# Kernel optimization log

Measured on AMD Instinct MI355X. Metric: run time of the kernel, lower is better.

## Reference

```python
import jax, jax.numpy as jnp
import numpy as np

N_NODES = 50000
N_EDGES = 800000
NUM_GRAPHS = 512
IN_DIM = 128
HID = 128
OUT_DIM = 1


def setup_inputs() -> dict:
    key = jax.random.key(0)
    ks = jax.random.split(key, 8)
    x = jax.random.normal(ks[0], (N_NODES, IN_DIM), dtype=jnp.float32)
    edge_index = jax.random.randint(ks[1], (2, N_EDGES), 0, N_NODES, dtype=jnp.int64)
    batch = jnp.sort(jax.random.randint(ks[2], (N_NODES,), 0, NUM_GRAPHS, dtype=jnp.int64))
    s1 = 1.0 / np.sqrt(IN_DIM)
    s2 = 1.0 / np.sqrt(HID)
    W1 = jax.random.normal(ks[3], (IN_DIM, HID), dtype=jnp.float32) * s1
    b1 = jnp.zeros((HID,), dtype=jnp.float32)
    W2 = jax.random.normal(ks[4], (HID, HID), dtype=jnp.float32) * s2
    b2 = jnp.zeros((HID,), dtype=jnp.float32)
    Wl = jax.random.normal(ks[5], (HID, OUT_DIM), dtype=jnp.float32) * s2
    bl = jnp.zeros((OUT_DIM,), dtype=jnp.float32)
    return {"x": x, "edge_index": edge_index, "batch": batch,
            "W1": W1, "b1": b1, "W2": W2, "b2": b2, "Wl": Wl, "bl": bl}


def _gcn_conv(x, src, dst, norm, W, b):
    # GCNConv: D^{-1/2}(A+I)D^{-1/2} X W + b (self-loops already in src/dst)
    h = x @ W                                    # [N, H]
    msg = h[src] * norm[:, None]                 # gather + edge-normalize
    agg = jax.ops.segment_sum(msg, dst, num_segments=N_NODES)  # scatter-add
    return agg + b


def reference(x, edge_index, batch, W1, b1, W2, b2, Wl, bl):
    loops = jnp.arange(N_NODES, dtype=edge_index.dtype)
    src = jnp.concatenate([edge_index[0], loops])
    dst = jnp.concatenate([edge_index[1], loops])
    deg = jax.ops.segment_sum(jnp.ones_like(dst, dtype=x.dtype), dst, num_segments=N_NODES)
    dinv = jax.lax.rsqrt(deg)                    # deg >= 1 due to self-loops
    norm = dinv[src] * dinv[dst]                 # symmetric normalization per edge

    h = jax.nn.relu(_gcn_conv(x, src, dst, norm, W1, b1))
    h = jax.nn.relu(_gcn_conv(h, src, dst, norm, W2, b2))

    # global_mean_pool over graph ids
    sums = jax.ops.segment_sum(h, batch, num_segments=NUM_GRAPHS)
    cnts = jax.ops.segment_sum(jnp.ones((N_NODES,), dtype=h.dtype), batch, num_segments=NUM_GRAPHS)
    pooled = sums / jnp.maximum(cnts, 1.0)[:, None]

    out = jax.nn.sigmoid(pooled @ Wl + bl)       # [G, 1]
    return out.squeeze(1)                        # [G]
```

## Files before the change

### kernel.cpp

```cpp
#include <hip/hip_runtime.h>
#include <hip/hip_bf16.h>

#define N_NODES 50000
#define N_EDGES 800000
#define NUM_GRAPHS 512
#define MAXDEG 64
#define EPB 4096
#define P1_BLOCKS 196
#define NBUCK 256
#define NPB 196

typedef short short8 __attribute__((ext_vector_type(8)));
typedef unsigned short u16x8 __attribute__((ext_vector_type(8)));
typedef float f32x4 __attribute__((ext_vector_type(4)));

__device__ __forceinline__ unsigned short f2bu(float f) {
    __hip_bfloat16 h = __float2bfloat16(f);
    return *reinterpret_cast<unsigned short*>(&h);
}
__device__ __forceinline__ float bu2f(unsigned short u) {
    unsigned int v = ((unsigned int)u) << 16;
    float f;
    __builtin_memcpy(&f, &v, 4);
    return f;
}

__global__ __launch_bounds__(256) void bin_k(const int* __restrict__ ei,
                                             unsigned int* __restrict__ staging,
                                             int* __restrict__ cnts_tbl,
                                             int* __restrict__ offs_tbl,
                                             unsigned short* __restrict__ hs1,
                                             unsigned short* __restrict__ hs2) {
    __shared__ unsigned int st[EPB];
    __shared__ int cnt[NBUCK], cur[NBUCK], scan[NBUCK];
    int b = blockIdx.x, t = threadIdx.x;
    if (b == 0 && t < 64)
        ((unsigned int*)(hs1 + (size_t)N_NODES * 128))[t] = 0u;
    if (b == 1 && t < 64)
        ((unsigned int*)(hs2 + (size_t)N_NODES * 128))[t] = 0u;
    cnt[t] = 0;
    __syncthreads();

    int e0 = b * EPB;
    int srcv[16], dstv[16], bk[16];
#pragma unroll
    for (int k = 0; k < 16; ++k) {
        int e = e0 + k * 256 + t;
        bool ok = e < N_EDGES;
        srcv[k] = ok ? ei[e] : 0;
        dstv[k] = ok ? ei[N_EDGES + e] : 0;
        bk[k] = ok ? (dstv[k] / NPB) : -1;
        if (ok) atomicAdd(&cnt[bk[k]], 1);
    }
    __syncthreads();
    scan[t] = cnt[t];
    __syncthreads();
    for (int off = 1; off < 256; off <<= 1) {
        int u = t >= off ? scan[t - off] : 0;
        __syncthreads();
        scan[t] += u;
        __syncthreads();
    }
    int excl = scan[t] - cnt[t];
    cur[t] = excl;
    cnts_tbl[t * P1_BLOCKS + b] = cnt[t];
    offs_tbl[t * P1_BLOCKS + b] = excl;
    __syncthreads();
#pragma unroll
    for (int k = 0; k < 16; ++k) {
        if (bk[k] >= 0) {
            int pos = atomicAdd(&cur[bk[k]], 1);
            int dl = dstv[k] - bk[k] * NPB;
            st[pos] = (unsigned int)srcv[k] | ((unsigned int)dl << 16);
        }
    }
    __syncthreads();
    unsigned int* gout = staging + (size_t)b * EPB;
    for (int i = t; i < EPB; i += 256) gout[i] = st[i];
}

__global__ __launch_bounds__(256) void adjbuild_k(const unsigned int* __restrict__ staging,
                                                  const int* __restrict__ cnts_tbl,
                                                  const int* __restrict__ offs_tbl,
                                                  unsigned short* __restrict__ adj,
                                                  int* __restrict__ cnt,
                                                  float* __restrict__ dinv,
                                                  const float* __restrict__ W1,
                                                  const float* __restrict__ W2,
                                                  unsigned short* __restrict__ W1t,
                                                  unsigned short* __restrict__ W2t) {
    int b = blockIdx.x, t = threadIdx.x;
    if (b >= NBUCK) {
        int wb = b - NBUCK;
        const float* W = wb < 64 ? W1 : W2;
        unsigned short* Wt = wb < 64 ? W1t : W2t;
        int idx = (wb & 63) * 256 + t;
        int k = idx >> 7, n = idx & 127;
        Wt[n * 128 + k] = f2bu(W[idx]);
        return;
    }
    __shared__ unsigned short adjL[NPB * MAXDEG];
    __shared__ int cntL[NPB];
    __shared__ int segStart[P1_BLOCKS + 1];
    __shared__ int segOff[P1_BLOCKS];
    __shared__ int tmp[256];

    if (t < NPB) cntL[t] = 0;
    int c = t < P1_BLOCKS ? cnts_tbl[b * P1_BLOCKS + t] : 0;
    if (t < P1_BLOCKS) segOff[t] = offs_tbl[b * P1_BLOCKS + t];
    tmp[t] = c;
    __syncthreads();
    for (int off = 1; off < 256; off <<= 1) {
        int u = t >= off ? tmp[t - off] : 0;
        __syncthreads();
        tmp[t] += u;
        __syncthreads();
    }
    if (t < P1_BLOCKS) segStart[t] = tmp[t] - c;
    if (t == 0) segStart[P1_BLOCKS] = tmp[P1_BLOCKS - 1];
    __syncthreads();

    int T = segStart[P1_BLOCKS];
    for (int f = t; f < T; f += 256) {
        int lo = 0, hi = P1_BLOCKS;
        while (hi - lo > 1) {
            int m = (lo + hi) >> 1;
            if (segStart[m] <= f) lo = m; else hi = m;
        }
        unsigned int p = staging[(size_t)lo * EPB + segOff[lo] + (f - segStart[lo])];
        int src = p & 0xFFFF;
        int dl = p >> 16;
        int slot = atomicAdd(&cntL[dl], 1);
        if (slot < MAXDEG - 1) adjL[dl * MAXDEG + slot] = (unsigned short)src;
    }
    __syncthreads();

    int nodeBase = b * NPB;
    if (t < NPB) {
        int node = nodeBase + t;
        int cc = cntL[t];
        int ec = cc < MAXDEG - 1 ? cc : MAXDEG - 1;
        adjL[t * MAXDEG + ec] = (unsigned short)node;
        int tot = ec + 1, tot4 = (tot + 3) & ~3;
        for (int s = tot; s < tot4; ++s) adjL[t * MAXDEG + s] = (unsigned short)N_NODES;
        if (node < N_NODES) {
            cnt[node] = cc;
            dinv[node] = rsqrtf((float)cc + 1.0f);
        }
    }
    __syncthreads();
    unsigned int* g = (unsigned int*)(adj + (size_t)nodeBase * MAXDEG);
    const unsigned int* l = (const unsigned int*)adjL;
    for (int i = t; i < NPB * MAXDEG / 2; i += 256) g[i] = l[i];
}

template <bool F32A>
__global__ __launch_bounds__(256) void gemm_k(const void* __restrict__ Ap,
                                              const unsigned short* __restrict__ Wt,
                                              const float* __restrict__ dinv,
                                              unsigned short* __restrict__ C) {
    __shared__ unsigned short Wl[128 * 136];
    int t = threadIdx.x;
    for (int idx = t; idx < 2048; idx += 256) {
        int n = idx >> 4, c = idx & 15;
        *(u16x8*)(Wl + n * 136 + c * 8) = *(const u16x8*)(Wt + n * 128 + c * 8);
    }
    __syncthreads();

    int wave = t >> 6, lane = t & 63, quad = lane >> 4, ln = lane & 15;
    int rb = blockIdx.x * 128 + wave * 16;

    short8 a[2][4];
#pragma unroll
    for (int mt = 0; mt < 2; ++mt) {
        int r = rb + mt * 64 + ln;
        r = r < N_NODES ? r : N_NODES - 1;
        if (F32A) {
            const float* arow = (const float*)Ap + (size_t)r * 128 + quad * 8;
#pragma unroll
            for (int ks = 0; ks < 4; ++ks) {
                float4 v0 = *(const float4*)(arow + ks * 32);
                float4 v1 = *(const float4*)(arow + ks * 32 + 4);
                short8 av;
                av[0] = (short)f2bu(v0.x); av[1] = (short)f2bu(v0.y);
                av[2] = (short)f2bu(v0.z); av[3] = (short)f2bu(v0.w);
                av[4] = (short)f2bu(v1.x); av[5] = (short)f2bu(v1.y);
                av[6] = (short)f2bu(v1.z); av[7] = (short)f2bu(v1.w);
                a[mt][ks] = av;
            }
        } else {
            const unsigned short* arow = (const unsigned short*)Ap + (size_t)r * 128 + quad * 8;
#pragma unroll
            for (int ks = 0; ks < 4; ++ks) a[mt][ks] = *(const short8*)(arow + ks * 32);
        }
    }

    f32x4 acc[2][8];
#pragma unroll
    for (int mt = 0; mt < 2; ++mt)
#pragma unroll
        for (int ct = 0; ct < 8; ++ct) acc[mt][ct] = (f32x4){0.f, 0.f, 0.f, 0.f};

#pragma unroll
    for (int ks = 0; ks < 4; ++ks)
#pragma unroll
        for (int ct = 0; ct < 8; ++ct) {
            short8 b = *(const short8*)(Wl + (ct * 16 + ln) * 136 + ks * 32 + quad * 8);
            acc[0][ct] = __builtin_amdgcn_mfma_f32_16x16x32_bf16(a[0][ks], b, acc[0][ct], 0, 0, 0);
            acc[1][ct] = __builtin_amdgcn_mfma_f32_16x16x32_bf16(a[1][ks], b, acc[1][ct], 0, 0, 0);
        }

#pragma unroll
    for (int mt = 0; mt < 2; ++mt) {
#pragma unroll
        for (int rr = 0; rr < 4; ++rr) {
            int r = rb + mt * 64 + quad * 4 + rr;
            if (r >= N_NODES) continue;
            float dv = dinv[r];
#pragma unroll
            for (int ct = 0; ct < 8; ++ct)
                C[(size_t)r * 128 + ct * 16 + ln] = f2bu(acc[mt][ct][rr] * dv);
        }
    }
}

__global__ __launch_bounds__(256) void agg1_k(const unsigned short* __restrict__ hs,
                                              const unsigned short* __restrict__ adj,
                                              const int* __restrict__ cnt,
                                              const float* __restrict__ dinv,
                                              const float* __restrict__ bias,
                                              unsigned short* __restrict__ out) {
    int wave = threadIdx.x >> 6, lane = threadIdx.x & 63;
    int node0 = blockIdx.x * 8 + wave * 2;
    int node1 = node0 + 1;
    int quad = lane >> 4, fl = lane & 15;
    int idx0 = (int)adj[node0 * MAXDEG + lane];
    int idx1 = (int)adj[node1 * MAXDEG + lane];
    int c0 = cnt[node0], c1 = cnt[node1];
    int ec0 = c0 < MAXDEG - 1 ? c0 : MAXDEG - 1;
    int ec1 = c1 < MAXDEG - 1 ? c1 : MAXDEG - 1;
    int it0 = (ec0 + 4) >> 2;
    int it1 = (ec1 + 4) >> 2;
    int common = it0 < it1 ? it0 : it1;

    float a0[8], a1[8];
#pragma unroll
    for (int j = 0; j < 8; ++j) { a0[j] = 0.f; a1[j] = 0.f; }

    int i = 0;
    for (; i + 2 <= common; i += 2) {
        int sA0 = __shfl(idx0, i * 4 + quad, 64);
        int sA1 = __shfl(idx0, i * 4 + 4 + quad, 64);
        int sB0 = __shfl(idx1, i * 4 + quad, 64);
        int sB1 = __shfl(idx1, i * 4 + 4 + quad, 64);
        u16x8 vA0 = *(const u16x8*)(hs + (size_t)sA0 * 128 + fl * 8);
        u16x8 vA1 = *(const u16x8*)(hs + (size_t)sA1 * 128 + fl * 8);
        u16x8 vB0 = *(const u16x8*)(hs + (size_t)sB0 * 128 + fl * 8);
        u16x8 vB1 = *(const u16x8*)(hs + (size_t)sB1 * 128 + fl * 8);
#pragma unroll
        for (int j = 0; j < 8; ++j) {
            a0[j] += bu2f(vA0[j]) + bu2f(vA1[j]);
            a1[j] += bu2f(vB0[j]) + bu2f(vB1[j]);
        }
    }
    for (; i < common; ++i) {
        int sA = __shfl(idx0, i * 4 + quad, 64);
        int sB = __shfl(idx1, i * 4 + quad, 64);
        u16x8 vA = *(const u16x8*)(hs + (size_t)sA * 128 + fl * 8);
        u16x8 vB = *(const u16x8*)(hs + (size_t)sB * 128 + fl * 8);
#pragma unroll
        for (int j = 0; j < 8; ++j) { a0[j] += bu2f(vA[j]); a1[j] += bu2f(vB[j]); }
    }
    for (; i < it0; ++i) {
        int sA = __shfl(idx0, i * 4 + quad, 64);
        u16x8 vA = *(const u16x8*)(hs + (size_t)sA * 128 + fl * 8);
#pragma unroll
        for (int j = 0; j < 8; ++j) a0[j] += bu2f(vA[j]);
    }
    for (; i < it1; ++i) {
        int sB = __shfl(idx1, i * 4 + quad, 64);
        u16x8 vB = *(const u16x8*)(hs + (size_t)sB * 128 + fl * 8);
#pragma unroll
        for (int j = 0; j < 8; ++j) a1[j] += bu2f(vB[j]);
    }

#pragma unroll
    for (int j = 0; j < 8; ++j) {
        a0[j] += __shfl_xor(a0[j], 16, 64);
        a0[j] += __shfl_xor(a0[j], 32, 64);
        a1[j] += __shfl_xor(a1[j], 16, 64);
        a1[j] += __shfl_xor(a1[j], 32, 64);
    }

    if (quad < 2) {
        int node = quad == 0 ? node0 : node1;
        const float* av = nullptr;
        float dv = dinv[node];
        float4 b0 = *(const float4*)(bias + fl * 8);
        float4 b1 = *(const float4*)(bias + fl * 8 + 4);
        float r0 = quad == 0 ? a0[0] : a1[0];
        float r1 = quad == 0 ? a0[1] : a1[1];
        float r2 = quad == 0 ? a0[2] : a1[2];
        float r3 = quad == 0 ? a0[3] : a1[3];
        float r4 = quad == 0 ? a0[4] : a1[4];
        float r5 = quad == 0 ? a0[5] : a1[5];
        float r6 = quad == 0 ? a0[6] : a1[6];
        float r7 = quad == 0 ? a0[7] : a1[7];
        u16x8 o;
        o[0] = f2bu(fmaxf(r0 * dv + b0.x, 0.f));
        o[1] = f2bu(fmaxf(r1 * dv + b0.y, 0.f));
        o[2] = f2bu(fmaxf(r2 * dv + b0.z, 0.f));
        o[3] = f2bu(fmaxf(r3 * dv + b0.w, 0.f));
        o[4] = f2bu(fmaxf(r4 * dv + b1.x, 0.f));
        o[5] = f2bu(fmaxf(r5 * dv + b1.y, 0.f));
        o[6] = f2bu(fmaxf(r6 * dv + b1.z, 0.f));
        o[7] = f2bu(fmaxf(r7 * dv + b1.w, 0.f));
        *(u16x8*)(out + (size_t)node * 128 + fl * 8) = o;
        (void)av;
    }
}

__global__ __launch_bounds__(256) void agg_dot_k(const unsigned short* __restrict__ hs,
                                                 const unsigned short* __restrict__ adj,
                                                 const int* __restrict__ cnt,
                                                 const float* __restrict__ dinv,
                                                 const float* __restrict__ bias,
                                                 const float* __restrict__ Wl,
                                                 float* __restrict__ pnode) {
    int wave = threadIdx.x >> 6, lane = threadIdx.x & 63;
    int node0 = blockIdx.x * 8 + wave * 2;
    int node1 = node0 + 1;
    int quad = lane >> 4, fl = lane & 15;
    int idx0 = (int)adj[node0 * MAXDEG + lane];
    int idx1 = (int)adj[node1 * MAXDEG + lane];
    int c0 = cnt[node0], c1 = cnt[node1];
    int ec0 = c0 < MAXDEG - 1 ? c0 : MAXDEG - 1;
    int ec1 = c1 < MAXDEG - 1 ? c1 : MAXDEG - 1;
    int it0 = (ec0 + 4) >> 2;
    int it1 = (ec1 + 4) >> 2;
    int common = it0 < it1 ? it0 : it1;

    float a0[8], a1[8];
#pragma unroll
    for (int j = 0; j < 8; ++j) { a0[j] = 0.f; a1[j] = 0.f; }

    int i = 0;
    for (; i + 2 <= common; i += 2) {
        int sA0 = __shfl(idx0, i * 4 + quad, 64);
        int sA1 = __shfl(idx0, i * 4 + 4 + quad, 64);
        int sB0 = __shfl(idx1, i * 4 + quad, 64);
        int sB1 = __shfl(idx1, i * 4 + 4 + quad, 64);
        u16x8 vA0 = *(const u16x8*)(hs + (size_t)sA0 * 128 + fl * 8);
        u16x8 vA1 = *(const u16x8*)(hs + (size_t)sA1 * 128 + fl * 8);
        u16x8 vB0 = *(const u16x8*)(hs + (size_t)sB0 * 128 + fl * 8);
        u16x8 vB1 = *(const u16x8*)(hs + (size_t)sB1 * 128 + fl * 8);
#pragma unroll
        for (int j = 0; j < 8; ++j) {
            a0[j] += bu2f(vA0[j]) + bu2f(vA1[j]);
            a1[j] += bu2f(vB0[j]) + bu2f(vB1[j]);
        }
    }
    for (; i < common; ++i) {
        int sA = __shfl(idx0, i * 4 + quad, 64);
        int sB = __shfl(idx1, i * 4 + quad, 64);
        u16x8 vA = *(const u16x8*)(hs + (size_t)sA * 128 + fl * 8);
        u16x8 vB = *(const u16x8*)(hs + (size_t)sB * 128 + fl * 8);
#pragma unroll
        for (int j = 0; j < 8; ++j) { a0[j] += bu2f(vA[j]); a1[j] += bu2f(vB[j]); }
    }
    for (; i < it0; ++i) {
        int sA = __shfl(idx0, i * 4 + quad, 64);
        u16x8 vA = *(const u16x8*)(hs + (size_t)sA * 128 + fl * 8);
#pragma unroll
        for (int j = 0; j < 8; ++j) a0[j] += bu2f(vA[j]);
    }
    for (; i < it1; ++i) {
        int sB = __shfl(idx1, i * 4 + quad, 64);
        u16x8 vB = *(const u16x8*)(hs + (size_t)sB * 128 + fl * 8);
#pragma unroll
        for (int j = 0; j < 8; ++j) a1[j] += bu2f(vB[j]);
    }

#pragma unroll
    for (int j = 0; j < 8; ++j) {
        a0[j] += __shfl_xor(a0[j], 16, 64);
        a0[j] += __shfl_xor(a0[j], 32, 64);
        a1[j] += __shfl_xor(a1[j], 16, 64);
        a1[j] += __shfl_xor(a1[j], 32, 64);
    }

    float dv0 = dinv[node0], dv1 = dinv[node1];
    float4 b0 = *(const float4*)(bias + fl * 8);
    float4 b1 = *(const float4*)(bias + fl * 8 + 4);
    float4 w0 = *(const float4*)(Wl + fl * 8);
    float4 w1 = *(const float4*)(Wl + fl * 8 + 4);
    float p0 = fmaxf(a0[0] * dv0 + b0.x, 0.f) * w0.x
             + fmaxf(a0[1] * dv0 + b0.y, 0.f) * w0.y
             + fmaxf(a0[2] * dv0 + b0.z, 0.f) * w0.z
             + fmaxf(a0[3] * dv0 + b0.w, 0.f) * w0.w
             + fmaxf(a0[4] * dv0 + b1.x, 0.f) * w1.x
             + fmaxf(a0[5] * dv0 + b1.y, 0.f) * w1.y
             + fmaxf(a0[6] * dv0 + b1.z, 0.f) * w1.z
             + fmaxf(a0[7] * dv0 + b1.w, 0.f) * w1.w;
    float p1 = fmaxf(a1[0] * dv1 + b0.x, 0.f) * w0.x
             + fmaxf(a1[1] * dv1 + b0.y, 0.f) * w0.y
             + fmaxf(a1[2] * dv1 + b0.z, 0.f) * w0.z
             + fmaxf(a1[3] * dv1 + b0.w, 0.f) * w0.w
             + fmaxf(a1[4] * dv1 + b1.x, 0.f) * w1.x
             + fmaxf(a1[5] * dv1 + b1.y, 0.f) * w1.y
             + fmaxf(a1[6] * dv1 + b1.z, 0.f) * w1.z
             + fmaxf(a1[7] * dv1 + b1.w, 0.f) * w1.w;
    p0 += __shfl_xor(p0, 1, 64);
    p0 += __shfl_xor(p0, 2, 64);
    p0 += __shfl_xor(p0, 4, 64);
    p0 += __shfl_xor(p0, 8, 64);
    p1 += __shfl_xor(p1, 1, 64);
    p1 += __shfl_xor(p1, 2, 64);
    p1 += __shfl_xor(p1, 4, 64);
    p1 += __shfl_xor(p1, 8, 64);
    if (lane == 0) {
        float2 pw; pw.x = p0; pw.y = p1;
        *(float2*)(pnode + node0) = pw;
    }
}

__device__ __forceinline__ int lb(const int* a, int n, int v) {
    int lo = 0, hi = n;
    while (lo < hi) {
        int m = (lo + hi) >> 1;
        if (a[m] < v) lo = m + 1;
        else hi = m;
    }
    return lo;
}

__global__ __launch_bounds__(64) void final_k(const float* __restrict__ pnode,
                                              const int* __restrict__ batch,
                                              const float* __restrict__ bl,
                                              float* __restrict__ out) {
    int g = blockIdx.x, t = threadIdx.x;
    int lo = lb(batch, N_NODES, g), hi = lb(batch, N_NODES, g + 1);
    float s = 0.f;
    for (int r = lo + t; r < hi; r += 64) s += pnode[r];
#pragma unroll
    for (int o = 32; o > 0; o >>= 1) s += __shfl_down(s, o, 64);
    if (t == 0) {
        float cf = (float)(hi - lo);
        float z = s / fmaxf(cf, 1.f) + bl[0];
        out[g] = 1.f / (1.f + expf(-z));
    }
}

extern "C" void kernel_launch(void* const* d_in, const int* in_sizes, int n_in,
                              void* d_out, int out_size, void* d_ws, size_t ws_size,
                              hipStream_t stream) {
    const float* x = (const float*)d_in[0];
    const int* ei = (const int*)d_in[1];
    const int* batch = (const int*)d_in[2];
    const float* W1 = (const float*)d_in[3];
    const float* b1 = (const float*)d_in[4];
    const float* W2 = (const float*)d_in[5];
    const float* b2 = (const float*)d_in[6];
    const float* Wl = (const float*)d_in[7];
    const float* bl = (const float*)d_in[8];
    float* out = (float*)d_out;

    char* ws = (char*)d_ws;
    unsigned int* staging = (unsigned int*)(ws + 0x0);
    int* cnts_tbl = (int*)(ws + 0x310000);
    int* offs_tbl = (int*)(ws + 0x341000);
    unsigned short* adj = (unsigned short*)(ws + 0x372000);
    int* cnt = (int*)(ws + 0x992000);
    float* dinv = (float*)(ws + 0x9C3000);
    unsigned short* W1t = (unsigned short*)(ws + 0x9F4000);
    unsigned short* W2t = (unsigned short*)(ws + 0x9FC000);
    float* pnode = (float*)(ws + 0xA04000);
    unsigned short* hs1 = (unsigned short*)(ws + 0xA36000);
    unsigned short* h1 = (unsigned short*)(ws + 0x1672000);
    unsigned short* hs2 = (unsigned short*)(ws + 0x22AE000);

    bin_k<<<P1_BLOCKS, 256, 0, stream>>>(ei, staging, cnts_tbl, offs_tbl, hs1, hs2);
    adjbuild_k<<<NBUCK + 128, 256, 0, stream>>>(staging, cnts_tbl, offs_tbl,
                                                adj, cnt, dinv, W1, W2, W1t, W2t);

    gemm_k<true><<<(N_NODES + 127) / 128, 256, 0, stream>>>(x, W1t, dinv, hs1);
    agg1_k<<<N_NODES / 8, 256, 0, stream>>>(hs1, adj, cnt, dinv, b1, h1);
    gemm_k<false><<<(N_NODES + 127) / 128, 256, 0, stream>>>(h1, W2t, dinv, hs2);
    agg_dot_k<<<N_NODES / 8, 256, 0, stream>>>(hs2, adj, cnt, dinv, b2, Wl, pnode);

    final_k<<<NUM_GRAPHS, 64, 0, stream>>>(pnode, batch, bl, out);
}
```

Measured before the change: 189.3 us.

## Reorder layer-2 as aggregate-then-GEMM and fuse W2 matmul into aggregation kernel

```diff
diff --git a/kernel.cpp b/kernel.cpp
--- a/kernel.cpp
+++ b/kernel.cpp
@@ -30,14 +30,14 @@
                                              int* __restrict__ cnts_tbl,
                                              int* __restrict__ offs_tbl,
                                              unsigned short* __restrict__ hs1,
-                                             unsigned short* __restrict__ hs2) {
+                                             unsigned short* __restrict__ h1s) {
     __shared__ unsigned int st[EPB];
     __shared__ int cnt[NBUCK], cur[NBUCK], scan[NBUCK];
     int b = blockIdx.x, t = threadIdx.x;
     if (b == 0 && t < 64)
         ((unsigned int*)(hs1 + (size_t)N_NODES * 128))[t] = 0u;
     if (b == 1 && t < 64)
-        ((unsigned int*)(hs2 + (size_t)N_NODES * 128))[t] = 0u;
+        ((unsigned int*)(h1s + (size_t)N_NODES * 128))[t] = 0u;
     cnt[t] = 0;
     __syncthreads();
 
@@ -154,8 +154,7 @@
     for (int i = t; i < NPB * MAXDEG / 2; i += 256) g[i] = l[i];
 }
 
-template <bool F32A>
-__global__ __launch_bounds__(256) void gemm_k(const void* __restrict__ Ap,
+__global__ __launch_bounds__(256) void gemm_k(const float* __restrict__ Ap,
                                               const unsigned short* __restrict__ Wt,
                                               const float* __restrict__ dinv,
                                               unsigned short* __restrict__ C) {
@@ -175,23 +174,17 @@
     for (int mt = 0; mt < 2; ++mt) {
         int r = rb + mt * 64 + ln;
         r = r < N_NODES ? r : N_NODES - 1;
-        if (F32A) {
-            const float* arow = (const float*)Ap + (size_t)r * 128 + quad * 8;
-#pragma unroll
-            for (int ks = 0; ks < 4; ++ks) {
-                float4 v0 = *(const float4*)(arow + ks * 32);
-                float4 v1 = *(const float4*)(arow + ks * 32 + 4);
-                short8 av;
-                av[0] = (short)f2bu(v0.x); av[1] = (short)f2bu(v0.y);
-                av[2] = (short)f2bu(v0.z); av[3] = (short)f2bu(v0.w);
-                av[4] = (short)f2bu(v1.x); av[5] = (short)f2bu(v1.y);
-                av[6] = (short)f2bu(v1.z); av[7] = (short)f2bu(v1.w);
-                a[mt][ks] = av;
-            }
-        } else {
-            const unsigned short* arow = (const unsigned short*)Ap + (size_t)r * 128 + quad * 8;
-#pragma unroll
-            for (int ks = 0; ks < 4; ++ks) a[mt][ks] = *(const short8*)(arow + ks * 32);
+        const float* arow = Ap + (size_t)r * 128 + quad * 8;
+#pragma unroll
+        for (int ks = 0; ks < 4; ++ks) {
+            float4 v0 = *(const float4*)(arow + ks * 32);
+            float4 v1 = *(const float4*)(arow + ks * 32 + 4);
+            short8 av;
+            av[0] = (short)f2bu(v0.x); av[1] = (short)f2bu(v0.y);
+            av[2] = (short)f2bu(v0.z); av[3] = (short)f2bu(v0.w);
+            av[4] = (short)f2bu(v1.x); av[5] = (short)f2bu(v1.y);
+            av[6] = (short)f2bu(v1.z); av[7] = (short)f2bu(v1.w);
+            a[mt][ks] = av;
         }
     }
 
@@ -294,7 +287,6 @@
 
     if (quad < 2) {
         int node = quad == 0 ? node0 : node1;
-        const float* av = nullptr;
         float dv = dinv[node];
         float4 b0 = *(const float4*)(bias + fl * 8);
         float4 b1 = *(const float4*)(bias + fl * 8 + 4);
@@ -307,30 +299,36 @@
         float r6 = quad == 0 ? a0[6] : a1[6];
         float r7 = quad == 0 ? a0[7] : a1[7];
         u16x8 o;
-        o[0] = f2bu(fmaxf(r0 * dv + b0.x, 0.f));
-        o[1] = f2bu(fmaxf(r1 * dv + b0.y, 0.f));
-        o[2] = f2bu(fmaxf(r2 * dv + b0.z, 0.f));
-        o[3] = f2bu(fmaxf(r3 * dv + b0.w, 0.f));
-        o[4] = f2bu(fmaxf(r4 * dv + b1.x, 0.f));
-        o[5] = f2bu(fmaxf(r5 * dv + b1.y, 0.f));
-        o[6] = f2bu(fmaxf(r6 * dv + b1.z, 0.f));
-        o[7] = f2bu(fmaxf(r7 * dv + b1.w, 0.f));
+        o[0] = f2bu(fmaxf(r0 * dv + b0.x, 0.f) * dv);
+        o[1] = f2bu(fmaxf(r1 * dv + b0.y, 0.f) * dv);
+        o[2] = f2bu(fmaxf(r2 * dv + b0.z, 0.f) * dv);
+        o[3] = f2bu(fmaxf(r3 * dv + b0.w, 0.f) * dv);
+        o[4] = f2bu(fmaxf(r4 * dv + b1.x, 0.f) * dv);
+        o[5] = f2bu(fmaxf(r5 * dv + b1.y, 0.f) * dv);
+        o[6] = f2bu(fmaxf(r6 * dv + b1.z, 0.f) * dv);
+        o[7] = f2bu(fmaxf(r7 * dv + b1.w, 0.f) * dv);
         *(u16x8*)(out + (size_t)node * 128 + fl * 8) = o;
-        (void)av;
-    }
-}
-
-__global__ __launch_bounds__(256) void agg_dot_k(const unsigned short* __restrict__ hs,
-                                                 const unsigned short* __restrict__ adj,
-                                                 const int* __restrict__ cnt,
-                                                 const float* __restrict__ dinv,
-                                                 const float* __restrict__ bias,
-                                                 const float* __restrict__ Wl,
-                                                 float* __restrict__ pnode) {
-    int wave = threadIdx.x >> 6, lane = threadIdx.x & 63;
-    int node0 = blockIdx.x * 8 + wave * 2;
-    int node1 = node0 + 1;
+    }
+}
+
+__global__ __launch_bounds__(256) void agg_w2_dot_k(const unsigned short* __restrict__ h1s,
+                                                    const unsigned short* __restrict__ adj,
+                                                    const int* __restrict__ cnt,
+                                                    const float* __restrict__ dinv,
+                                                    const float* __restrict__ b2,
+                                                    const float* __restrict__ Wl,
+                                                    const unsigned short* __restrict__ W2t,
+                                                    float* __restrict__ pnode) {
+    __shared__ unsigned short tA[16 * 136];
+    __shared__ float part[8][4];
+    int t = threadIdx.x, wave = t >> 6, lane = t & 63;
     int quad = lane >> 4, fl = lane & 15;
+    int nb = blockIdx.x * 8;
+    int node0 = nb + wave * 2, node1 = node0 + 1;
+
+    for (int i = t; i < 544; i += 256)
+        ((unsigned int*)(tA + 8 * 136))[i] = 0u;
+
     int idx0 = (int)adj[node0 * MAXDEG + lane];
     int idx1 = (int)adj[node1 * MAXDEG + lane];
     int c0 = cnt[node0], c1 = cnt[node1];
@@ -350,10 +348,10 @@
         int sA1 = __shfl(idx0, i * 4 + 4 + quad, 64);
         int sB0 = __shfl(idx1, i * 4 + quad, 64);
         int sB1 = __shfl(idx1, i * 4 + 4 + quad, 64);
-        u16x8 vA0 = *(const u16x8*)(hs + (size_t)sA0 * 128 + fl * 8);
-        u16x8 vA1 = *(const u16x8*)(hs + (size_t)sA1 * 128 + fl * 8);
-        u16x8 vB0 = *(const u16x8*)(hs + (size_t)sB0 * 128 + fl * 8);
-        u16x8 vB1 = *(const u16x8*)(hs + (size_t)sB1 * 128 + fl * 8);
+        u16x8 vA0 = *(const u16x8*)(h1s + (size_t)sA0 * 128 + fl * 8);
+        u16x8 vA1 = *(const u16x8*)(h1s + (size_t)sA1 * 128 + fl * 8);
+        u16x8 vB0 = *(const u16x8*)(h1s + (size_t)sB0 * 128 + fl * 8);
+        u16x8 vB1 = *(const u16x8*)(h1s + (size_t)sB1 * 128 + fl * 8);
 #pragma unroll
         for (int j = 0; j < 8; ++j) {
             a0[j] += bu2f(vA0[j]) + bu2f(vA1[j]);
@@ -363,20 +361,20 @@
     for (; i < common; ++i) {
         int sA = __shfl(idx0, i * 4 + quad, 64);
         int sB = __shfl(idx1, i * 4 + quad, 64);
-        u16x8 vA = *(const u16x8*)(hs + (size_t)sA * 128 + fl * 8);
-        u16x8 vB = *(const u16x8*)(hs + (size_t)sB * 128 + fl * 8);
+        u16x8 vA = *(const u16x8*)(h1s + (size_t)sA * 128 + fl * 8);
+        u16x8 vB = *(const u16x8*)(h1s + (size_t)sB * 128 + fl * 8);
 #pragma unroll
         for (int j = 0; j < 8; ++j) { a0[j] += bu2f(vA[j]); a1[j] += bu2f(vB[j]); }
     }
     for (; i < it0; ++i) {
         int sA = __shfl(idx0, i * 4 + quad, 64);
-        u16x8 vA = *(const u16x8*)(hs + (size_t)sA * 128 + fl * 8);
+        u16x8 vA = *(const u16x8*)(h1s + (size_t)sA * 128 + fl * 8);
 #pragma unroll
         for (int j = 0; j < 8; ++j) a0[j] += bu2f(vA[j]);
     }
     for (; i < it1; ++i) {
         int sB = __shfl(idx1, i * 4 + quad, 64);
-        u16x8 vB = *(const u16x8*)(hs + (size_t)sB * 128 + fl * 8);
+        u16x8 vB = *(const u16x8*)(h1s + (size_t)sB * 128 + fl * 8);
 #pragma unroll
         for (int j = 0; j < 8; ++j) a1[j] += bu2f(vB[j]);
     }
@@ -389,39 +387,58 @@
         a1[j] += __shfl_xor(a1[j], 32, 64);
     }
 
-    float dv0 = dinv[node0], dv1 = dinv[node1];
-    float4 b0 = *(const float4*)(bias + fl * 8);
-    float4 b1 = *(const float4*)(bias + fl * 8 + 4);
-    float4 w0 = *(const float4*)(Wl + fl * 8);
-    float4 w1 = *(const float4*)(Wl + fl * 8 + 4);
-    float p0 = fmaxf(a0[0] * dv0 + b0.x, 0.f) * w0.x
-             + fmaxf(a0[1] * dv0 + b0.y, 0.f) * w0.y
-             + fmaxf(a0[2] * dv0 + b0.z, 0.f) * w0.z
-             + fmaxf(a0[3] * dv0 + b0.w, 0.f) * w0.w
-             + fmaxf(a0[4] * dv0 + b1.x, 0.f) * w1.x
-             + fmaxf(a0[5] * dv0 + b1.y, 0.f) * w1.y
-             + fmaxf(a0[6] * dv0 + b1.z, 0.f) * w1.z
-             + fmaxf(a0[7] * dv0 + b1.w, 0.f) * w1.w;
-    float p1 = fmaxf(a1[0] * dv1 + b0.x, 0.f) * w0.x
-             + fmaxf(a1[1] * dv1 + b0.y, 0.f) * w0.y
-             + fmaxf(a1[2] * dv1 + b0.z, 0.f) * w0.z
-             + fmaxf(a1[3] * dv1 + b0.w, 0.f) * w0.w
-             + fmaxf(a1[4] * dv1 + b1.x, 0.f) * w1.x
-             + fmaxf(a1[5] * dv1 + b1.y, 0.f) * w1.y
-             + fmaxf(a1[6] * dv1 + b1.z, 0.f) * w1.z
-             + fmaxf(a1[7] * dv1 + b1.w, 0.f) * w1.w;
-    p0 += __shfl_xor(p0, 1, 64);
-    p0 += __shfl_xor(p0, 2, 64);
-    p0 += __shfl_xor(p0, 4, 64);
-    p0 += __shfl_xor(p0, 8, 64);
-    p1 += __shfl_xor(p1, 1, 64);
-    p1 += __shfl_xor(p1, 2, 64);
-    p1 += __shfl_xor(p1, 4, 64);
-    p1 += __shfl_xor(p1, 8, 64);
-    if (lane == 0) {
-        float2 pw; pw.x = p0; pw.y = p1;
-        *(float2*)(pnode + node0) = pw;
-    }
+    if (quad < 2) {
+        u16x8 o;
+#pragma unroll
+        for (int j = 0; j < 8; ++j) o[j] = f2bu(quad == 0 ? a0[j] : a1[j]);
+        *(u16x8*)(tA + (wave * 2 + quad) * 136 + fl * 8) = o;
+    }
+    __syncthreads();
+
+    int ln = fl;
+    short8 af[4];
+#pragma unroll
+    for (int ks = 0; ks < 4; ++ks)
+        af[ks] = *(const short8*)(tA + ln * 136 + ks * 32 + quad * 8);
+
+    f32x4 acc2[2];
+    acc2[0] = (f32x4){0.f, 0.f, 0.f, 0.f};
+    acc2[1] = (f32x4){0.f, 0.f, 0.f, 0.f};
+#pragma unroll
+    for (int ks = 0; ks < 4; ++ks)
+#pragma unroll
+        for (int ct = 0; ct < 2; ++ct) {
+            short8 bf = *(const short8*)(W2t + (size_t)(wave * 32 + ct * 16 + ln) * 128 + ks * 32 + quad * 8);
+            acc2[ct] = __builtin_amdgcn_mfma_f32_16x16x32_bf16(af[ks], bf, acc2[ct], 0, 0, 0);
+        }
+
+    float dvr[4];
+#pragma unroll
+    for (int rr = 0; rr < 4; ++rr) {
+        int nidx = nb + quad * 4 + rr;
+        nidx = nidx < N_NODES ? nidx : N_NODES - 1;
+        dvr[rr] = dinv[nidx];
+    }
+    float b2v[2], wlv[2];
+#pragma unroll
+    for (int ct = 0; ct < 2; ++ct) {
+        int col = wave * 32 + ct * 16 + ln;
+        b2v[ct] = b2[col];
+        wlv[ct] = Wl[col];
+    }
+#pragma unroll
+    for (int rr = 0; rr < 4; ++rr) {
+        float v = fmaxf(dvr[rr] * acc2[0][rr] + b2v[0], 0.f) * wlv[0]
+                + fmaxf(dvr[rr] * acc2[1][rr] + b2v[1], 0.f) * wlv[1];
+        v += __shfl_xor(v, 1, 64);
+        v += __shfl_xor(v, 2, 64);
+        v += __shfl_xor(v, 4, 64);
+        v += __shfl_xor(v, 8, 64);
+        if (quad < 2 && fl == 0) part[quad * 4 + rr][wave] = v;
+    }
+    __syncthreads();
+    if (t < 8)
+        pnode[nb + t] = (part[t][0] + part[t][1]) + (part[t][2] + part[t][3]);
 }
 
 __device__ __forceinline__ int lb(const int* a, int n, int v) {
@@ -476,17 +493,15 @@
     unsigned short* W2t = (unsigned short*)(ws + 0x9FC000);
     float* pnode = (float*)(ws + 0xA04000);
     unsigned short* hs1 = (unsigned short*)(ws + 0xA36000);
-    unsigned short* h1 = (unsigned short*)(ws + 0x1672000);
-    unsigned short* hs2 = (unsigned short*)(ws + 0x22AE000);
-
-    bin_k<<<P1_BLOCKS, 256, 0, stream>>>(ei, staging, cnts_tbl, offs_tbl, hs1, hs2);
+    unsigned short* h1s = (unsigned short*)(ws + 0x1672000);
+
+    bin_k<<<P1_BLOCKS, 256, 0, stream>>>(ei, staging, cnts_tbl, offs_tbl, hs1, h1s);
     adjbuild_k<<<NBUCK + 128, 256, 0, stream>>>(staging, cnts_tbl, offs_tbl,
                                                 adj, cnt, dinv, W1, W2, W1t, W2t);
 
-    gemm_k<true><<<(N_NODES + 127) / 128, 256, 0, stream>>>(x, W1t, dinv, hs1);
-    agg1_k<<<N_NODES / 8, 256, 0, stream>>>(hs1, adj, cnt, dinv, b1, h1);
-    gemm_k<false><<<(N_NODES + 127) / 128, 256, 0, stream>>>(h1, W2t, dinv, hs2);
-    agg_dot_k<<<N_NODES / 8, 256, 0, stream>>>(hs2, adj, cnt, dinv, b2, Wl, pnode);
+    gemm_k<<<(N_NODES + 127) / 128, 256, 0, stream>>>(x, W1t, dinv, hs1);
+    agg1_k<<<N_NODES / 8, 256, 0, stream>>>(hs1, adj, cnt, dinv, b1, h1s);
+    agg_w2_dot_k<<<N_NODES / 8, 256, 0, stream>>>(h1s, adj, cnt, dinv, b2, Wl, W2t, pnode);
 
     final_k<<<NUM_GRAPHS, 64, 0, stream>>>(pnode, batch, bl, out);
 }
```

After: 198.5 us. +4.9%, slower.
